# Kernel tuning notes

Hardware: AMD Instinct MI355X
Metric: run time of the kernel (lower is better)

Reference implementation:

```python
import jax, jax.numpy as jnp
import numpy as np

N = 50000      # nodes
E = 800000     # edges
H, C = 4, 32   # heads, per-head channels
NF = 513       # n_fft//2 + 1 frequency bins
NMEL = 128
NEG_SLOPE_ATT = 0.2   # GATConv leaky_relu slope
NEG_SLOPE_MLP = 0.01  # F.leaky_relu default


def setup_inputs() -> dict:
    key = jax.random.key(0)
    ks = jax.random.split(key, 12)
    s = 0.05
    return {
        "x": jax.random.normal(ks[0], (N, NF), jnp.float32),
        "edge_index": jax.random.randint(ks[1], (2, E), 0, N, dtype=jnp.int32),
        "fb": jax.random.normal(ks[2], (NF, NMEL), jnp.float32) * s,
        "Wg": jax.random.normal(ks[3], (NMEL, H * C), jnp.float32) * s,
        "bias_g": jnp.zeros((H * C,), jnp.float32),
        "att_src": jax.random.normal(ks[4], (H, C), jnp.float32) * s,
        "att_dst": jax.random.normal(ks[5], (H, C), jnp.float32) * s,
        "W1": jax.random.normal(ks[6], (H * C, 256), jnp.float32) * s,
        "b1": jnp.zeros((256,), jnp.float32),
        "W2": jax.random.normal(ks[7], (256, 128), jnp.float32) * s,
        "b2": jnp.zeros((128,), jnp.float32),
        "W3": jax.random.normal(ks[8], (128, 10), jnp.float32) * s,
        "b3": jnp.zeros((10,), jnp.float32),
    }


def gat_conv(h, src, dst, att_src, att_dst, bias_g):
    # h: [N, H, C]; per-edge attention, segment softmax over dst, scatter-add
    a_s = jnp.einsum('nhc,hc->nh', h, att_src)  # [N, H]
    a_d = jnp.einsum('nhc,hc->nh', h, att_dst)  # [N, H]
    e = jax.nn.leaky_relu(a_s[src] + a_d[dst], NEG_SLOPE_ATT)  # [E', H]
    m = jax.ops.segment_max(e, dst, num_segments=N)            # [N, H]
    ex = jnp.exp(e - m[dst])
    denom = jax.ops.segment_sum(ex, dst, num_segments=N)       # [N, H]
    alpha = ex / denom[dst]                                    # [E', H]
    msg = h[src] * alpha[:, :, None]                           # [E', H, C]
    out = jax.ops.segment_sum(msg, dst, num_segments=N)        # [N, H, C]
    return out.reshape(N, H * C) + bias_g


def reference(x, edge_index, fb, Wg, bias_g, att_src, att_dst, W1, b1, W2, b2, W3, b3):
    # learnable mel filterbank projection: [N, NF] -> [N, NMEL]
    x = x @ fb
    # GATConv linear transform, split into heads
    h = (x @ Wg).reshape(N, H, C)
    # add self loops (PyG GATConv default add_self_loops=True)
    loop = jnp.arange(N, dtype=edge_index.dtype)
    src = jnp.concatenate([edge_index[0], loop])
    dst = jnp.concatenate([edge_index[1], loop])
    x = jax.nn.elu(gat_conv(h, src, dst, att_src, att_dst, bias_g))
    # dropout is identity in eval mode
    x = jax.nn.leaky_relu(x @ W1 + b1, NEG_SLOPE_MLP)
    x = jax.nn.leaky_relu(x @ W2 + b2, NEG_SLOPE_MLP)
    x = jax.nn.leaky_relu(x @ W3 + b3, NEG_SLOPE_MLP)
    return jax.nn.softmax(x, axis=-1)
```

## Files before the change

### kernel.cpp

```cpp
#include <hip/hip_runtime.h>
#include <hip/hip_bf16.h>

#define NN 50000
#define EE 800000
#define NFR 513
#define NMEL 128
#define HC 128

typedef __bf16 bf16x8 __attribute__((ext_vector_type(8)));
typedef float floatx4 __attribute__((ext_vector_type(4)));

struct __attribute__((packed, aligned(4))) u4a { unsigned x, y, z, w; };

__device__ __forceinline__ unsigned short f2b(float f) {
    unsigned u = __float_as_uint(f);
    u = (u + 0x7FFFu + ((u >> 16) & 1u)) >> 16;
    return (unsigned short)u;
}
__device__ __forceinline__ unsigned short f2bu(unsigned u) {
    u = (u + 0x7FFFu + ((u >> 16) & 1u)) >> 16;
    return (unsigned short)u;
}
__device__ __forceinline__ float b2f(unsigned short s) {
    return __uint_as_float(((unsigned)s) << 16);
}
__device__ __forceinline__ float lexp(float a) {
    a = a > 0.f ? a : 0.2f * a;
    return __expf(a);
}

__device__ __forceinline__ float ldf(const float* p, long i) { return p[i]; }
__device__ __forceinline__ void stf(float* p, long i, float v) { p[i] = v; }
__device__ __forceinline__ void stf(__hip_bfloat16* p, long i, float v) {
    ((unsigned short*)p)[i] = f2b(v);
}

#define BM 64
#define BN 64
#define BK 16

template<int EPI, typename TA, typename TB, typename TC>
__global__ __launch_bounds__(256) void gemm_k(const TA* __restrict__ A, const TB* __restrict__ B,
                                              TC* __restrict__ C, int M, int Nn, int K,
                                              const float* __restrict__ bias)
{
    __shared__ float As[BK][BM + 4];
    __shared__ float Bs[BK][BN + 4];
    const int t = threadIdx.x;
    const int row0 = blockIdx.x * BM;
    const int col0 = blockIdx.y * BN;
    const int tc = t & 15, tr = t >> 4;
    float acc[4][4] = {};

    for (int kb = 0; kb < K; kb += BK) {
        #pragma unroll
        for (int i = 0; i < 4; ++i) {
            int idx = i * 256 + t;
            int r = idx >> 4, k = idx & 15;
            int gr = row0 + r, gk = kb + k;
            float v = 0.f;
            if (gr < M && gk < K) v = ldf(A, (long)gr * K + gk);
            As[k][r] = v;
        }
        #pragma unroll
        for (int i = 0; i < 4; ++i) {
            int idx = i * 256 + t;
            int c = idx & 63, k = idx >> 6;
            int gk = kb + k, gc = col0 + c;
            float v = 0.f;
            if (gk < K && gc < Nn) v = ldf(B, (long)gk * Nn + gc);
            Bs[k][c] = v;
        }
        __syncthreads();
        #pragma unroll
        for (int kk = 0; kk < BK; ++kk) {
            float4 av = *reinterpret_cast<const float4*>(&As[kk][tr << 2]);
            float4 bv = *reinterpret_cast<const float4*>(&Bs[kk][tc << 2]);
            float a[4] = {av.x, av.y, av.z, av.w};
            float b[4] = {bv.x, bv.y, bv.z, bv.w};
            #pragma unroll
            for (int i = 0; i < 4; ++i)
                #pragma unroll
                for (int j = 0; j < 4; ++j)
                    acc[i][j] += a[i] * b[j];
        }
        __syncthreads();
    }

    #pragma unroll
    for (int i = 0; i < 4; ++i) {
        int gr = row0 + (tr << 2) + i;
        if (gr >= M) continue;
        #pragma unroll
        for (int j = 0; j < 4; ++j) {
            int gc = col0 + (tc << 2) + j;
            if (gc >= Nn) continue;
            float v = acc[i][j];
            if (EPI == 2) {
                stf(C, (long)gc * 544 + gr, v);
            } else {
                if (EPI == 1) { v += bias[gc]; v = v > 0.f ? v : 0.01f * v; }
                stf(C, (long)gr * Nn + gc, v);
            }
        }
    }
}

__global__ void k_trans(const float* __restrict__ in, __hip_bfloat16* __restrict__ outp,
                        int K, int N, int KP)
{
    int id = blockIdx.x * 256 + threadIdx.x;
    if (id >= N * KP) return;
    int n = id / KP, k = id % KP;
    float v = (k < K) ? in[(long)k * N + n] : 0.f;
    ((unsigned short*)outp)[id] = f2b(v);
}

#define PS 40

template<typename T> struct ARegs;
template<> struct ARegs<float> { unsigned v[8]; };
template<> struct ARegs<__hip_bfloat16> { uint4 v; };

__device__ __forceinline__ void loadA_r(const float* __restrict__ A, ARegs<float>& r, int t,
                                        int row0, int M, int K, int kb)
{
    #pragma unroll
    for (int g = 0; g < 2; ++g) {
        int q = g * 256 + t;
        int row = q >> 3, k4 = (q & 7) * 4;
        int gr = row0 + row, gk = kb + k4;
        unsigned f0 = 0, f1 = 0, f2 = 0, f3 = 0;
        if (gr < M) {
            const float* ap = A + (long)gr * K + gk;
            if (gk + 3 < K) {
                u4a u = *reinterpret_cast<const u4a*>(ap);
                f0 = u.x; f1 = u.y; f2 = u.z; f3 = u.w;
            } else {
                if (gk + 0 < K) f0 = __float_as_uint(ap[0]);
                if (gk + 1 < K) f1 = __float_as_uint(ap[1]);
                if (gk + 2 < K) f2 = __float_as_uint(ap[2]);
            }
        }
        r.v[g * 4 + 0] = f0; r.v[g * 4 + 1] = f1;
        r.v[g * 4 + 2] = f2; r.v[g * 4 + 3] = f3;
    }
}

__device__ __forceinline__ void writeA_r(unsigned short* As, const ARegs<float>& r, int t)
{
    #pragma unroll
    for (int g = 0; g < 2; ++g) {
        int q = g * 256 + t;
        int row = q >> 3, k4 = (q & 7) * 4;
        ushort4 pk;
        pk.x = f2bu(r.v[g * 4 + 0]); pk.y = f2bu(r.v[g * 4 + 1]);
        pk.z = f2bu(r.v[g * 4 + 2]); pk.w = f2bu(r.v[g * 4 + 3]);
        *reinterpret_cast<ushort4*>(&As[row * PS + k4]) = pk;
    }
}

__device__ __forceinline__ void loadA_r(const __hip_bfloat16* __restrict__ A, ARegs<__hip_bfloat16>& r,
                                        int t, int row0, int M, int K, int kb)
{
    int row = t >> 2, k8 = (t & 3) * 8;
    int gr = row0 + row;
    uint4 val = make_uint4(0, 0, 0, 0);
    if (gr < M) val = *reinterpret_cast<const uint4*>(A + (long)gr * K + kb + k8);
    r.v = val;
}

__device__ __forceinline__ void writeA_r(unsigned short* As, const ARegs<__hip_bfloat16>& r, int t)
{
    int row = t >> 2, k8 = (t & 3) * 8;
    *reinterpret_cast<uint4*>(&As[row * PS + k8]) = r.v;
}

__device__ __forceinline__ void loadB_r(const __hip_bfloat16* __restrict__ Bt, uint4* bR, int t,
                                        int col0, int Nn, int KB, int kb)
{
    #pragma unroll
    for (int g = 0; g < 2; ++g) {
        int c = g * 256 + t;
        int row = c >> 2, k8 = (c & 3) * 8;
        int gn = col0 + row;
        uint4 val = make_uint4(0, 0, 0, 0);
        if (gn < Nn) val = *reinterpret_cast<const uint4*>(Bt + (long)gn * KB + kb + k8);
        bR[g] = val;
    }
}

__device__ __forceinline__ void writeB_r(unsigned short* Bs, const uint4* bR, int t)
{
    #pragma unroll
    for (int g = 0; g < 2; ++g) {
        int c = g * 256 + t;
        int row = c >> 2, k8 = (c & 3) * 8;
        *reinterpret_cast<uint4*>(&Bs[row * PS + k8]) = bR[g];
    }
}

template<int EPI, typename TA, typename TC>
__global__ __launch_bounds__(256) void mgemm(const TA* __restrict__ A,
                                             const __hip_bfloat16* __restrict__ Bt,
                                             TC* __restrict__ C,
                                             int M, int Nn, int K, int KB,
                                             const float* __restrict__ bias,
                                             const float* __restrict__ pf1,
                                             const float* __restrict__ pf2,
                                             float* __restrict__ po1,
                                             float* __restrict__ po2)
{
    __shared__ unsigned short As[2][64 * PS];
    __shared__ unsigned short Bs[2][128 * PS];
    __shared__ unsigned short x2s[(EPI == 3) ? 64 * 130 : 2];
    __shared__ float w3s[(EPI == 3) ? 1280 : 1];

    const int t = threadIdx.x;
    const int row0 = blockIdx.x * 64;
    const int col0 = blockIdx.y * 128;
    const int wave = t >> 6, lane = t & 63;
    const int wm = (wave >> 1) * 32, wn = (wave & 1) * 64;
    const int lm = lane & 15, kq = lane >> 4;

    if (EPI == 3) {
        for (int i = t; i < 1280; i += 256) w3s[i] = pf1[i];
    }

    floatx4 acc[2][4];
    #pragma unroll
    for (int i = 0; i < 2; ++i)
        #pragma unroll
        for (int j = 0; j < 4; ++j)
            acc[i][j] = 0.f;

    ARegs<TA> aR;
    uint4 bR[2];
    loadA_r(A, aR, t, row0, M, K, 0);
    loadB_r(Bt, bR, t, col0, Nn, KB, 0);

    const int nIter = KB >> 5;
    int b = 0;
    for (int it = 0; it < nIter; ++it) {
        writeA_r(As[b], aR, t);
        writeB_r(Bs[b], bR, t);
        if (it + 1 < nIter) {
            loadA_r(A, aR, t, row0, M, K, (it + 1) * 32);
            loadB_r(Bt, bR, t, col0, Nn, KB, (it + 1) * 32);
        }
        asm volatile("s_waitcnt lgkmcnt(0)" ::: "memory");
        __builtin_amdgcn_s_barrier();
        __builtin_amdgcn_sched_barrier(0);

        bf16x8 af[2], bf[4];
        #pragma unroll
        for (int i = 0; i < 2; ++i)
            af[i] = *reinterpret_cast<const bf16x8*>(&As[b][(wm + i * 16 + lm) * PS + kq * 8]);
        #pragma unroll
        for (int j = 0; j < 4; ++j)
            bf[j] = *reinterpret_cast<const bf16x8*>(&Bs[b][(wn + j * 16 + lm) * PS + kq * 8]);
        #pragma unroll
        for (int i = 0; i < 2; ++i)
            #pragma unroll
            for (int j = 0; j < 4; ++j)
                acc[i][j] = __builtin_amdgcn_mfma_f32_16x16x32_bf16(af[i], bf[j], acc[i][j], 0, 0, 0);
        b ^= 1;
    }

    #pragma unroll
    for (int i = 0; i < 2; ++i) {
        #pragma unroll
        for (int r = 0; r < 4; ++r) {
            int lrow = wm + i * 16 + kq * 4 + r;
            int gr = row0 + lrow;
            if (gr >= M) continue;
            #pragma unroll
            for (int j = 0; j < 4; ++j) {
                int gc = col0 + wn + j * 16 + lm;
                float v = acc[i][j][r];
                if (EPI == 1 || EPI == 3) { v += bias[gc]; v = v > 0.f ? v : 0.01f * v; }
                if (EPI == 3) x2s[lrow * 130 + gc] = f2b(v);
                else stf(C, (long)gr * Nn + gc, v);
            }
        }
    }

    if (EPI == 4) {
        float wsv[4], wdv[4];
        #pragma unroll
        for (int j = 0; j < 4; ++j) {
            int gc = wn + j * 16 + lm;
            wsv[j] = pf1[gc];
            wdv[j] = pf2[gc];
        }
        #pragma unroll
        for (int i = 0; i < 2; ++i) {
            #pragma unroll
            for (int r = 0; r < 4; ++r) {
                float s0 = acc[i][0][r] * wsv[0] + acc[i][1][r] * wsv[1];
                float s1 = acc[i][2][r] * wsv[2] + acc[i][3][r] * wsv[3];
                float d0 = acc[i][0][r] * wdv[0] + acc[i][1][r] * wdv[1];
                float d1 = acc[i][2][r] * wdv[2] + acc[i][3][r] * wdv[3];
                #pragma unroll
                for (int m = 1; m < 16; m <<= 1) {
                    s0 += __shfl_xor(s0, m); s1 += __shfl_xor(s1, m);
                    d0 += __shfl_xor(d0, m); d1 += __shfl_xor(d1, m);
                }
                if (lm == 0) {
                    int grow = row0 + wm + i * 16 + kq * 4 + r;
                    if (grow < M) {
                        int h0 = wn >> 5;
                        po1[grow * 4 + h0]     = s0;
                        po1[grow * 4 + h0 + 1] = s1;
                        po2[grow * 4 + h0]     = d0;
                        po2[grow * 4 + h0 + 1] = d1;
                    }
                }
            }
        }
    }

    if (EPI == 3) {
        __syncthreads();
        if (t < 64) {
            int grow = row0 + t;
            if (grow < M) {
                float l[10];
                #pragma unroll
                for (int j = 0; j < 10; ++j) l[j] = pf2[j];
                #pragma unroll 8
                for (int c = 0; c < 128; ++c) {
                    float xv = b2f(x2s[t * 130 + c]);
                    const float* wr = &w3s[c * 10];
                    #pragma unroll
                    for (int j = 0; j < 10; ++j) l[j] += xv * wr[j];
                }
                float m = -1e30f;
                #pragma unroll
                for (int j = 0; j < 10; ++j) {
                    float v = l[j];
                    v = v > 0.f ? v : 0.01f * v;
                    l[j] = v;
                    m = fmaxf(m, v);
                }
                float sum = 0.f;
                #pragma unroll
                for (int j = 0; j < 10; ++j) { l[j] = __expf(l[j] - m); sum += l[j]; }
                float inv = 1.f / sum;
                #pragma unroll
                for (int j = 0; j < 10; ++j) po1[(long)grow * 10 + j] = l[j] * inv;
            }
        }
    }
}

__global__ void k_hist(const int* __restrict__ ei, int* __restrict__ hist)
{
    int e = blockIdx.x * 256 + threadIdx.x;
    if (e < EE) atomicAdd(&hist[ei[EE + e]], 1);
}

__global__ __launch_bounds__(512) void k_scan1(const int* __restrict__ hist, int* __restrict__ start,
                                               int* __restrict__ aux)
{
    __shared__ int sm[512];
    int t = threadIdx.x, i = blockIdx.x * 512 + t;
    int v = (i < NN) ? hist[i] : 0;
    sm[t] = v;
    __syncthreads();
    for (int off = 1; off < 512; off <<= 1) {
        int x = (t >= off) ? sm[t - off] : 0;
        __syncthreads();
        sm[t] += x;
        __syncthreads();
    }
    if (i < NN) start[i] = sm[t] - v;
    if (t == 511) aux[blockIdx.x] = sm[511];
}

__global__ void k_scan2(int* __restrict__ aux, int nb)
{
    int l = threadIdx.x;
    int v0 = (l < nb) ? aux[l] : 0;
    int v1 = (64 + l < nb) ? aux[64 + l] : 0;
    int s0 = v0, s1 = v1;
    for (int off = 1; off < 64; off <<= 1) {
        int u0 = __shfl_up(s0, off);
        int u1 = __shfl_up(s1, off);
        if (l >= off) { s0 += u0; s1 += u1; }
    }
    int tot0 = __shfl(s0, 63);
    if (l < nb) aux[l] = s0 - v0;
    if (64 + l < nb) aux[64 + l] = tot0 + s1 - v1;
}

__global__ __launch_bounds__(512) void k_scan3(int* __restrict__ start, int* __restrict__ cursor,
                                               const int* __restrict__ aux)
{
    int i = blockIdx.x * 512 + threadIdx.x;
    if (i < NN) {
        int v = start[i] + aux[blockIdx.x];
        start[i] = v;
        cursor[i] = v;
    }
    if (i == 0) start[NN] = EE;
}

__global__ void k_fill(const int* __restrict__ ei, int* __restrict__ cursor, int* __restrict__ sorted)
{
    int e = blockIdx.x * 256 + threadIdx.x;
    if (e >= EE) return;
    int s = ei[e], d = ei[EE + e];
    int pos = atomicAdd(&cursor[d], 1);
    sorted[pos] = s;
}

__global__ __launch_bounds__(256) void k_agg(const int* __restrict__ start, const int* __restrict__ sorted,
                                             const float* __restrict__ a_s, const float* __restrict__ a_d,
                                             const __hip_bfloat16* __restrict__ h,
                                             const float* __restrict__ bias_g,
                                             __hip_bfloat16* __restrict__ agg)
{
    int wave = threadIdx.x >> 6;
    int lane = threadIdx.x & 63;
    int d = blockIdx.x * 4 + wave;
    if (d >= NN) return;
    int hh = lane >> 4;
    float ad = a_d[d * 4 + hh];
    int e0 = start[d], e1 = start[d + 1];

    float ex = lexp(a_s[d * 4 + hh] + ad);
    unsigned hv = *reinterpret_cast<const unsigned*>(h + (long)d * HC + 2 * lane);
    float acc0 = ex * __uint_as_float(hv << 16);
    float acc1 = ex * __uint_as_float(hv & 0xffff0000u);
    float dsum = ex;

    int e = e0;
    for (; e + 4 <= e1; e += 4) {
        int s0 = sorted[e + 0], s1 = sorted[e + 1], s2 = sorted[e + 2], s3 = sorted[e + 3];
        float as0 = a_s[s0 * 4 + hh], as1 = a_s[s1 * 4 + hh];
        float as2 = a_s[s2 * 4 + hh], as3 = a_s[s3 * 4 + hh];
        unsigned h0 = *reinterpret_cast<const unsigned*>(h + (long)s0 * HC + 2 * lane);
        unsigned h1 = *reinterpret_cast<const unsigned*>(h + (long)s1 * HC + 2 * lane);
        unsigned h2 = *reinterpret_cast<const unsigned*>(h + (long)s2 * HC + 2 * lane);
        unsigned h3 = *reinterpret_cast<const unsigned*>(h + (long)s3 * HC + 2 * lane);
        float x0 = lexp(as0 + ad), x1 = lexp(as1 + ad), x2 = lexp(as2 + ad), x3 = lexp(as3 + ad);
        acc0 += x0 * __uint_as_float(h0 << 16);
        acc1 += x0 * __uint_as_float(h0 & 0xffff0000u);
        acc0 += x1 * __uint_as_float(h1 << 16);
        acc1 += x1 * __uint_as_float(h1 & 0xffff0000u);
        acc0 += x2 * __uint_as_float(h2 << 16);
        acc1 += x2 * __uint_as_float(h2 & 0xffff0000u);
        acc0 += x3 * __uint_as_float(h3 << 16);
        acc1 += x3 * __uint_as_float(h3 & 0xffff0000u);
        dsum += x0 + x1 + x2 + x3;
    }
    for (; e < e1; ++e) {
        int s = sorted[e];
        float xe = lexp(a_s[s * 4 + hh] + ad);
        unsigned hs = *reinterpret_cast<const unsigned*>(h + (long)s * HC + 2 * lane);
        acc0 += xe * __uint_as_float(hs << 16);
        acc1 += xe * __uint_as_float(hs & 0xffff0000u);
        dsum += xe;
    }

    float inv = 1.f / dsum;
    float2 bg = *reinterpret_cast<const float2*>(bias_g + 2 * lane);
    float v0 = acc0 * inv + bg.x;
    float v1 = acc1 * inv + bg.y;
    v0 = v0 > 0.f ? v0 : expm1f(v0);
    v1 = v1 > 0.f ? v1 : expm1f(v1);
    unsigned pk = (unsigned)f2b(v0) | ((unsigned)f2b(v1) << 16);
    *reinterpret_cast<unsigned*>((unsigned short*)agg + (long)d * HC + 2 * lane) = pk;
}

extern "C" void kernel_launch(void* const* d_in, const int* in_sizes, int n_in,
                              void* d_out, int out_size, void* d_ws, size_t ws_size,
                              hipStream_t stream)
{
    const float* x       = (const float*)d_in[0];
    const int*   ei      = (const int*)d_in[1];
    const float* fb      = (const float*)d_in[2];
    const float* Wg      = (const float*)d_in[3];
    const float* bias_g  = (const float*)d_in[4];
    const float* att_src = (const float*)d_in[5];
    const float* att_dst = (const float*)d_in[6];
    const float* W1      = (const float*)d_in[7];
    const float* b1      = (const float*)d_in[8];
    const float* W2      = (const float*)d_in[9];
    const float* b2      = (const float*)d_in[10];
    const float* W3      = (const float*)d_in[11];
    const float* b3      = (const float*)d_in[12];
    float* out = (float*)d_out;
    float* ws = (float*)d_ws;

    float* a_s = ws + 0;
    float* a_d = ws + 200000;
    __hip_bfloat16* fbWgT = (__hip_bfloat16*)(ws + 400000);
    __hip_bfloat16* W1T   = (__hip_bfloat16*)(ws + 434816);
    __hip_bfloat16* W2T   = (__hip_bfloat16*)(ws + 451200);
    int* hist   = (int*)(ws + 467584);
    int* startA = (int*)(ws + 517584);
    int* aux    = (int*)(ws + 567588);
    int* sorted = (int*)(ws + 567720);
    __hip_bfloat16* hbufB = (__hip_bfloat16*)(ws + 1367720);
    __hip_bfloat16* aggB  = (__hip_bfloat16*)(ws + 4567720);
    __hip_bfloat16* x1B   = (__hip_bfloat16*)(ws + 7767720);
    int* cursor = hist;
    __hip_bfloat16* x2B = hbufB;
    if (ws_size < (size_t)14167720 * sizeof(float)) return;

    hipMemsetAsync(ws + 400000, 0, (size_t)117584 * sizeof(float), stream);

    gemm_k<2, float, float, __hip_bfloat16><<<dim3(9, 2), 256, 0, stream>>>(fb, Wg, fbWgT, NFR, HC, NMEL, nullptr);
    k_trans<<<128, 256, 0, stream>>>(W1, W1T, 128, 256, 128);
    k_trans<<<128, 256, 0, stream>>>(W2, W2T, 256, 128, 256);

    mgemm<4, float, __hip_bfloat16><<<dim3(782, 1), 256, 0, stream>>>(
        x, fbWgT, hbufB, NN, HC, NFR, 544, nullptr, att_src, att_dst, a_s, a_d);

    k_hist<<<(EE + 255) / 256, 256, 0, stream>>>(ei, hist);
    k_scan1<<<98, 512, 0, stream>>>(hist, startA, aux);
    k_scan2<<<1, 64, 0, stream>>>(aux, 98);
    k_scan3<<<98, 512, 0, stream>>>(startA, cursor, aux);
    k_fill<<<(EE + 255) / 256, 256, 0, stream>>>(ei, cursor, sorted);

    k_agg<<<(NN + 3) / 4, 256, 0, stream>>>(startA, sorted, a_s, a_d, hbufB, bias_g, aggB);

    mgemm<1, __hip_bfloat16, __hip_bfloat16><<<dim3(782, 2), 256, 0, stream>>>(
        aggB, W1T, x1B, NN, 256, 128, 128, b1, nullptr, nullptr, nullptr, nullptr);

    mgemm<3, __hip_bfloat16, __hip_bfloat16><<<dim3(782, 1), 256, 0, stream>>>(
        x1B, W2T, x2B, NN, 128, 256, 256, b2, W3, b3, out, nullptr);
}
```

Measured before the change: 408.9 us.

## Fuse W1, W2 and W3 MLP layers into a single kernel via LDS

Replaces the two separate MLP GEMM launches with one kernel that computes the 256-wide hidden layer for a 64-row tile into shared memory and then runs the second GEMM and the final 10-way projection plus softmax from LDS. This removes the global write and read of the intermediate x1 activation (50000x256 bf16) and one kernel launch. The cost is more LDS per block (around 50KB), which may reduce occupancy. The W1 pass is also serialized over two column halves per block, where it used to be split across two grid columns.

Measured after the change: 400.7 us. -2.0%, faster.

```diff
diff --git a/kernel.cpp b/kernel.cpp
--- a/kernel.cpp
+++ b/kernel.cpp
@@ -213,8 +213,6 @@
 {
     __shared__ unsigned short As[2][64 * PS];
     __shared__ unsigned short Bs[2][128 * PS];
-    __shared__ unsigned short x2s[(EPI == 3) ? 64 * 130 : 2];
-    __shared__ float w3s[(EPI == 3) ? 1280 : 1];
 
     const int t = threadIdx.x;
     const int row0 = blockIdx.x * 64;
@@ -222,10 +220,6 @@
     const int wave = t >> 6, lane = t & 63;
     const int wm = (wave >> 1) * 32, wn = (wave & 1) * 64;
     const int lm = lane & 15, kq = lane >> 4;
-
-    if (EPI == 3) {
-        for (int i = t; i < 1280; i += 256) w3s[i] = pf1[i];
-    }
 
     floatx4 acc[2][4];
     #pragma unroll
@@ -271,16 +265,14 @@
     for (int i = 0; i < 2; ++i) {
         #pragma unroll
         for (int r = 0; r < 4; ++r) {
-            int lrow = wm + i * 16 + kq * 4 + r;
-            int gr = row0 + lrow;
+            int gr = row0 + wm + i * 16 + kq * 4 + r;
             if (gr >= M) continue;
             #pragma unroll
             for (int j = 0; j < 4; ++j) {
                 int gc = col0 + wn + j * 16 + lm;
                 float v = acc[i][j][r];
-                if (EPI == 1 || EPI == 3) { v += bias[gc]; v = v > 0.f ? v : 0.01f * v; }
-                if (EPI == 3) x2s[lrow * 130 + gc] = f2b(v);
-                else stf(C, (long)gr * Nn + gc, v);
+                if (EPI == 1) { v += bias[gc]; v = v > 0.f ? v : 0.01f * v; }
+                stf(C, (long)gr * Nn + gc, v);
             }
         }
     }
@@ -319,37 +311,162 @@
             }
         }
     }
-
-    if (EPI == 3) {
-        __syncthreads();
-        if (t < 64) {
-            int grow = row0 + t;
-            if (grow < M) {
-                float l[10];
+}
+
+__global__ __launch_bounds__(256) void k_mlp(const __hip_bfloat16* __restrict__ A,
+                                             const __hip_bfloat16* __restrict__ W1t,
+                                             const __hip_bfloat16* __restrict__ W2t,
+                                             const float* __restrict__ b1,
+                                             const float* __restrict__ b2,
+                                             const float* __restrict__ W3,
+                                             const float* __restrict__ b3,
+                                             float* __restrict__ out, int M)
+{
+    __shared__ unsigned short As[2][64 * PS];
+    __shared__ unsigned short Bs[2][128 * PS];
+    __shared__ unsigned short x1s[64 * 264];
+    __shared__ float w3s[1280];
+
+    const int t = threadIdx.x;
+    const int row0 = blockIdx.x * 64;
+    const int wave = t >> 6, lane = t & 63;
+    const int wm = (wave >> 1) * 32, wn = (wave & 1) * 64;
+    const int lm = lane & 15, kq = lane >> 4;
+
+    for (int i = t; i < 1280; i += 256) w3s[i] = W3[i];
+
+    ARegs<__hip_bfloat16> aR;
+    uint4 bR[2];
+
+    #pragma unroll 1
+    for (int cp = 0; cp < 2; ++cp) {
+        floatx4 acc[2][4];
+        #pragma unroll
+        for (int i = 0; i < 2; ++i)
+            #pragma unroll
+            for (int j = 0; j < 4; ++j) acc[i][j] = 0.f;
+
+        loadA_r(A, aR, t, row0, M, 128, 0);
+        loadB_r(W1t, bR, t, cp * 128, 256, 128, 0);
+        int b = 0;
+        #pragma unroll 1
+        for (int it = 0; it < 4; ++it) {
+            writeA_r(As[b], aR, t);
+            writeB_r(Bs[b], bR, t);
+            if (it + 1 < 4) {
+                loadA_r(A, aR, t, row0, M, 128, (it + 1) * 32);
+                loadB_r(W1t, bR, t, cp * 128, 256, 128, (it + 1) * 32);
+            }
+            asm volatile("s_waitcnt lgkmcnt(0)" ::: "memory");
+            __builtin_amdgcn_s_barrier();
+            __builtin_amdgcn_sched_barrier(0);
+
+            bf16x8 af[2], bf[4];
+            #pragma unroll
+            for (int i = 0; i < 2; ++i)
+                af[i] = *reinterpret_cast<const bf16x8*>(&As[b][(wm + i * 16 + lm) * PS + kq * 8]);
+            #pragma unroll
+            for (int j = 0; j < 4; ++j)
+                bf[j] = *reinterpret_cast<const bf16x8*>(&Bs[b][(wn + j * 16 + lm) * PS + kq * 8]);
+            #pragma unroll
+            for (int i = 0; i < 2; ++i)
                 #pragma unroll
-                for (int j = 0; j < 10; ++j) l[j] = pf2[j];
-                #pragma unroll 8
-                for (int c = 0; c < 128; ++c) {
-                    float xv = b2f(x2s[t * 130 + c]);
-                    const float* wr = &w3s[c * 10];
-                    #pragma unroll
-                    for (int j = 0; j < 10; ++j) l[j] += xv * wr[j];
+                for (int j = 0; j < 4; ++j)
+                    acc[i][j] = __builtin_amdgcn_mfma_f32_16x16x32_bf16(af[i], bf[j], acc[i][j], 0, 0, 0);
+            b ^= 1;
+        }
+        #pragma unroll
+        for (int i = 0; i < 2; ++i)
+            #pragma unroll
+            for (int r = 0; r < 4; ++r) {
+                int lrow = wm + i * 16 + kq * 4 + r;
+                #pragma unroll
+                for (int j = 0; j < 4; ++j) {
+                    int gc = cp * 128 + wn + j * 16 + lm;
+                    float v = acc[i][j][r] + b1[gc];
+                    v = v > 0.f ? v : 0.01f * v;
+                    x1s[lrow * 264 + gc] = f2b(v);
                 }
-                float m = -1e30f;
+            }
+    }
+
+    loadB_r(W2t, bR, t, 0, 128, 256, 0);
+    __syncthreads();
+
+    floatx4 acc[2][4];
+    #pragma unroll
+    for (int i = 0; i < 2; ++i)
+        #pragma unroll
+        for (int j = 0; j < 4; ++j) acc[i][j] = 0.f;
+
+    int b = 0;
+    #pragma unroll 1
+    for (int it = 0; it < 8; ++it) {
+        writeB_r(Bs[b], bR, t);
+        if (it + 1 < 8) loadB_r(W2t, bR, t, 0, 128, 256, (it + 1) * 32);
+        asm volatile("s_waitcnt lgkmcnt(0)" ::: "memory");
+        __builtin_amdgcn_s_barrier();
+        __builtin_amdgcn_sched_barrier(0);
+
+        bf16x8 af[2], bf[4];
+        #pragma unroll
+        for (int i = 0; i < 2; ++i)
+            af[i] = *reinterpret_cast<const bf16x8*>(&x1s[(wm + i * 16 + lm) * 264 + it * 32 + kq * 8]);
+        #pragma unroll
+        for (int j = 0; j < 4; ++j)
+            bf[j] = *reinterpret_cast<const bf16x8*>(&Bs[b][(wn + j * 16 + lm) * PS + kq * 8]);
+        #pragma unroll
+        for (int i = 0; i < 2; ++i)
+            #pragma unroll
+            for (int j = 0; j < 4; ++j)
+                acc[i][j] = __builtin_amdgcn_mfma_f32_16x16x32_bf16(af[i], bf[j], acc[i][j], 0, 0, 0);
+        b ^= 1;
+    }
+
+    __syncthreads();
+    unsigned short* x2s = x1s;
+    #pragma unroll
+    for (int i = 0; i < 2; ++i)
+        #pragma unroll
+        for (int r = 0; r < 4; ++r) {
+            int lrow = wm + i * 16 + kq * 4 + r;
+            #pragma unroll
+            for (int j = 0; j < 4; ++j) {
+                int gc = wn + j * 16 + lm;
+                float v = acc[i][j][r] + b2[gc];
+                v = v > 0.f ? v : 0.01f * v;
+                x2s[lrow * 130 + gc] = f2b(v);
+            }
+        }
+    __syncthreads();
+
+    if (t < 64) {
+        int grow = row0 + t;
+        if (grow < M) {
+            float l[10];
+            #pragma unroll
+            for (int j = 0; j < 10; ++j) l[j] = b3[j];
+            #pragma unroll 8
+            for (int c = 0; c < 128; ++c) {
+                float xv = b2f(x2s[t * 130 + c]);
+                const float* wr = &w3s[c * 10];
                 #pragma unroll
-                for (int j = 0; j < 10; ++j) {
-                    float v = l[j];
-                    v = v > 0.f ? v : 0.01f * v;
-                    l[j] = v;
-                    m = fmaxf(m, v);
-                }
-                float sum = 0.f;
-                #pragma unroll
-                for (int j = 0; j < 10; ++j) { l[j] = __expf(l[j] - m); sum += l[j]; }
-                float inv = 1.f / sum;
-                #pragma unroll
-                for (int j = 0; j < 10; ++j) po1[(long)grow * 10 + j] = l[j] * inv;
-            }
+                for (int j = 0; j < 10; ++j) l[j] += xv * wr[j];
+            }
+            float m = -1e30f;
+            #pragma unroll
+            for (int j = 0; j < 10; ++j) {
+                float v = l[j];
+                v = v > 0.f ? v : 0.01f * v;
+                l[j] = v;
+                m = fmaxf(m, v);
+            }
+            float sum = 0.f;
+            #pragma unroll
+            for (int j = 0; j < 10; ++j) { l[j] = __expf(l[j] - m); sum += l[j]; }
+            float inv = 1.f / sum;
+            #pragma unroll
+            for (int j = 0; j < 10; ++j) out[(long)grow * 10 + j] = l[j] * inv;
         }
     }
 }
@@ -505,9 +622,7 @@
     int* sorted = (int*)(ws + 567720);
     __hip_bfloat16* hbufB = (__hip_bfloat16*)(ws + 1367720);
     __hip_bfloat16* aggB  = (__hip_bfloat16*)(ws + 4567720);
-    __hip_bfloat16* x1B   = (__hip_bfloat16*)(ws + 7767720);
     int* cursor = hist;
-    __hip_bfloat16* x2B = hbufB;
     if (ws_size < (size_t)14167720 * sizeof(float)) return;
 
     hipMemsetAsync(ws + 400000, 0, (size_t)117584 * sizeof(float), stream);
@@ -527,9 +642,5 @@
 
     k_agg<<<(NN + 3) / 4, 256, 0, stream>>>(startA, sorted, a_s, a_d, hbufB, bias_g, aggB);
 
-    mgemm<1, __hip_bfloat16, __hip_bfloat16><<<dim3(782, 2), 256, 0, stream>>>(
-        aggB, W1T, x1B, NN, 256, 128, 128, b1, nullptr, nullptr, nullptr, nullptr);
-
-    mgemm<3, __hip_bfloat16, __hip_bfloat16><<<dim3(782, 1), 256, 0, stream>>>(
-        x1B, W2T, x2B, NN, 128, 256, 256, b2, W3, b3, out, nullptr);
-}
+    k_mlp<<<782, 256, 0, stream>>>(aggB, W1T, W2T, b1, b2, W3, b3, out, NN);
+}
```
